# Optimization experiments

Measured on AMD Instinct MI355X. Metric: run time of the kernel, lower is better.

## Reference

```python
import jax, jax.numpy as jnp
import numpy as np

H = 1024
EPS = 1e-5
N_ENT = 1000
TOP_K = 5


def _ln(x, g, b):
    mu = jnp.mean(x, axis=-1, keepdims=True)
    var = jnp.mean((x - mu) ** 2, axis=-1, keepdims=True)
    return (x - mu) * jax.lax.rsqrt(var + EPS) * g + b


def _gelu(x):
    return jax.nn.gelu(x, approximate=False)  # torch nn.GELU default (erf)


def setup_inputs() -> dict:
    key = jax.random.key(0)
    ks = jax.random.split(key, 24)
    s = 0.02
    inp = {
        'hidden_states': jax.random.normal(ks[0], (8, 2048, H), jnp.float32),
        'entity_embeddings': jax.random.normal(ks[1], (N_ENT, H), jnp.float32) * 0.01,
        # entity_encoder: H -> 2H -> H -> LN
        'ee_w1': jax.random.normal(ks[2], (H, 2 * H), jnp.float32) * s,
        'ee_b1': jnp.zeros((2 * H,), jnp.float32),
        'ee_w2': jax.random.normal(ks[3], (2 * H, H), jnp.float32) * s,
        'ee_b2': jnp.zeros((H,), jnp.float32),
        'ee_g': jnp.ones((H,), jnp.float32),
        'ee_beta': jnp.zeros((H,), jnp.float32),
        # relation_encoder: H -> H -> H -> LN
        're_w1': jax.random.normal(ks[4], (H, H), jnp.float32) * s,
        're_b1': jnp.zeros((H,), jnp.float32),
        're_w2': jax.random.normal(ks[5], (H, H), jnp.float32) * s,
        're_b2': jnp.zeros((H,), jnp.float32),
        're_g': jnp.ones((H,), jnp.float32),
        're_beta': jnp.zeros((H,), jnp.float32),
        # reasoning_network: 3H -> 2H -> H -> LN
        'rn_w1': jax.random.normal(ks[6], (3 * H, 2 * H), jnp.float32) * s,
        'rn_b1': jnp.zeros((2 * H,), jnp.float32),
        'rn_w2': jax.random.normal(ks[7], (2 * H, H), jnp.float32) * s,
        'rn_b2': jnp.zeros((H,), jnp.float32),
        'rn_g': jnp.ones((H,), jnp.float32),
        'rn_beta': jnp.zeros((H,), jnp.float32),
        # validation_network: H -> H/2 -> 1 -> sigmoid
        'vn_w1': jax.random.normal(ks[8], (H, H // 2), jnp.float32) * s,
        'vn_b1': jnp.zeros((H // 2,), jnp.float32),
        'vn_w2': jax.random.normal(ks[9], (H // 2, 1), jnp.float32) * s,
        'vn_b2': jnp.zeros((1,), jnp.float32),
    }
    return inp


def reference(hidden_states, entity_embeddings,
              ee_w1, ee_b1, ee_w2, ee_b2, ee_g, ee_beta,
              re_w1, re_b1, re_w2, re_b2, re_g, re_beta,
              rn_w1, rn_b1, rn_w2, rn_b2, rn_g, rn_beta,
              vn_w1, vn_b1, vn_w2, vn_b2):
    # entity encoder over all tokens: [B,S,H]
    entity_features = _ln(_gelu(hidden_states @ ee_w1 + ee_b1) @ ee_w2 + ee_b2, ee_g, ee_beta)

    # query=None path: relation encoder on mean-pooled hidden states [B,H]
    pooled = jnp.mean(hidden_states, axis=1)
    relation_features = _ln(_gelu(pooled @ re_w1 + re_b1) @ re_w2 + re_b2, re_g, re_beta)
    query_features = relation_features

    # similarity + top-k entity retrieval
    entity_similarities = query_features @ entity_embeddings.T  # [B, N_ENT]
    top_values, top_indices = jax.lax.top_k(entity_similarities, TOP_K)
    retrieved_entities = entity_embeddings[top_indices]  # [B, K, H]

    # reasoning input: [mean retrieved entity | relation | mean context]
    entity_vec = jnp.mean(retrieved_entities, axis=1)  # [B,H]
    context_vec = jnp.mean(hidden_states, axis=1)      # [B,H]
    reasoning_in = jnp.concatenate([entity_vec, relation_features, context_vec], axis=-1)  # [B,3H]
    reasoning_output = _ln(_gelu(reasoning_in @ rn_w1 + rn_b1) @ rn_w2 + rn_b2, rn_g, rn_beta)

    validation_scores = jax.nn.sigmoid(_gelu(reasoning_output @ vn_w1 + vn_b1) @ vn_w2 + vn_b2)

    return (entity_features, relation_features, retrieved_entities,
            entity_similarities, top_indices, reasoning_output, validation_scores)
```

## Files before the change

kernel.cpp:

```cpp
#include <hip/hip_runtime.h>
#include <math.h>

#define H 1024
#define SEQ 2048
#define BATCH 8
#define N_ENT 1000
#define TOPK 5
#define LN_EPS 1e-5f

using bf16x8 = __attribute__((ext_vector_type(8))) __bf16;
using f32x4  = __attribute__((ext_vector_type(4))) float;
#define AS1 __attribute__((address_space(1)))
#define AS3 __attribute__((address_space(3)))


__device__ __forceinline__ float gelu_fast(float x) {
    float z = fabsf(x) * 0.70710678118654752440f;
    float t = __builtin_amdgcn_rcpf(fmaf(0.3275911f, z, 1.0f));
    float p = fmaf(fmaf(fmaf(fmaf(1.061405429f, t, -1.453152027f), t, 1.421413741f),
                        t, -0.284496736f), t, 0.254829592f) * t;
    float e = __builtin_amdgcn_exp2f(-z * z * 1.44269504088896f);
    float erfz = fmaf(-p, e, 1.0f);
    float s = copysignf(erfz, x);
    return 0.5f * x * (1.0f + s);
}

__device__ __forceinline__ float sigmoidf_(float x) {
    return 1.0f / (1.0f + expf(-x));
}

__device__ __forceinline__ unsigned short f2bf(float f) {
    unsigned int u = __float_as_uint(f);
    unsigned int r = (u + 0x7fffu + ((u >> 16) & 1u)) >> 16;
    return (unsigned short)r;
}

__device__ float block_sum(float v, float* red) {
    for (int off = 32; off > 0; off >>= 1) v += __shfl_down(v, off, 64);
    int wid = threadIdx.x >> 6;
    int lane = threadIdx.x & 63;
    int nw = blockDim.x >> 6;
    if (lane == 0) red[wid] = v;
    __syncthreads();
    if (threadIdx.x == 0) {
        float s = 0.f;
        for (int i = 0; i < nw; ++i) s += red[i];
        red[0] = s;
    }
    __syncthreads();
    float r = red[0];
    __syncthreads();
    return r;
}


__global__ void f2bf_kernel(const float* __restrict__ in, unsigned short* __restrict__ out, int n) {
    int i = (blockIdx.x * blockDim.x + threadIdx.x) * 4;
    if (i >= n) return;
    float4 v = *(const float4*)(in + i);
    ushort4 o;
    o.x = f2bf(v.x); o.y = f2bf(v.y); o.z = f2bf(v.z); o.w = f2bf(v.w);
    *(ushort4*)(out + i) = o;
}

__global__ void transpose_both_kernel(const float* __restrict__ w1, unsigned short* __restrict__ o1,
                                      const float* __restrict__ w2, unsigned short* __restrict__ o2) {
    __shared__ float tile[32][33];
    int bid = blockIdx.x;
    const float* in; unsigned short* out; int R, C, bx, by;
    if (bid < 2048) { in = w1; out = o1; R = 1024; C = 2048; bx = bid & 63; by = bid >> 6; }
    else { bid -= 2048; in = w2; out = o2; R = 2048; C = 1024; bx = bid & 31; by = bid >> 5; }
    int c0 = bx * 32, r0 = by * 32;
    int tx = threadIdx.x & 31, ty = threadIdx.x >> 5;
#pragma unroll
    for (int i = 0; i < 32; i += 8)
        tile[ty + i][tx] = in[(size_t)(r0 + ty + i) * C + c0 + tx];
    __syncthreads();
#pragma unroll
    for (int i = 0; i < 32; i += 8)
        out[(size_t)(c0 + ty + i) * R + r0 + tx] = f2bf(tile[tx][ty + i]);
}


__global__ void pool1_kernel(const float* __restrict__ hs, float* __restrict__ part,
                             unsigned short* __restrict__ hsb) {
    int sc = blockIdx.x, b = blockIdx.y, t = threadIdx.x;
    size_t rowbase = (size_t)b * SEQ + sc * 64;
    const float* p = hs + rowbase * H + t * 4;
    float4 a = {0.f, 0.f, 0.f, 0.f};
    for (int s = 0; s < 64; ++s) {
        float4 v = *(const float4*)(p + (size_t)s * H);
        a.x += v.x; a.y += v.y; a.z += v.z; a.w += v.w;
        if (hsb) {
            ushort4 o;
            o.x = f2bf(v.x); o.y = f2bf(v.y); o.z = f2bf(v.z); o.w = f2bf(v.w);
            *(ushort4*)(hsb + (rowbase + s) * H + t * 4) = o;
        }
    }
    *(float4*)(part + ((size_t)b * 32 + sc) * H + t * 4) = a;
}

__global__ void pool2_kernel(const float* __restrict__ part, float* __restrict__ pooled) {
    int b = blockIdx.x, t = threadIdx.x;
    float4 s = {0.f, 0.f, 0.f, 0.f};
    for (int sc = 0; sc < 32; ++sc) {
        float4 v = *(const float4*)(part + ((size_t)b * 32 + sc) * H + t * 4);
        s.x += v.x; s.y += v.y; s.z += v.z; s.w += v.w;
    }
    float4 o = {s.x * (1.0f / SEQ), s.y * (1.0f / SEQ), s.z * (1.0f / SEQ), s.w * (1.0f / SEQ)};
    *(float4*)(pooled + (size_t)b * H + t * 4) = o;
}


template <int KRANGE>
__global__ void mlp_partial_kernel(const float* __restrict__ X, int ldx,
                                   const float* __restrict__ W, int N,
                                   float* __restrict__ part) {
    __shared__ float xs[8][KRANGE];
    int jb = blockIdx.x, ks = blockIdx.y, t = threadIdx.x;
    int k0 = ks * KRANGE;
    for (int i = t; i < 8 * KRANGE; i += 256) {
        int b = i / KRANGE, k = i % KRANGE;
        xs[b][k] = X[(size_t)b * ldx + k0 + k];
    }
    __syncthreads();
    int j = jb * 256 + t;
    float acc[8] = {};
    for (int k = 0; k < KRANGE; ++k) {
        float w = W[(size_t)(k0 + k) * N + j];
#pragma unroll
        for (int b = 0; b < 8; ++b) acc[b] = fmaf(xs[b][k], w, acc[b]);
    }
#pragma unroll
    for (int b = 0; b < 8; ++b) part[((size_t)(ks * 8 + b)) * N + j] = acc[b];
}

template <int KRANGE>
__global__ void mlp_partial_fused_kernel(const float* __restrict__ Pprev, int ldp, int nksp,
                                         const float* __restrict__ b1,
                                         const float* __restrict__ W, int N,
                                         float* __restrict__ part) {
    __shared__ float xs[8][KRANGE];
    int jb = blockIdx.x, ks = blockIdx.y, t = threadIdx.x;
    int k0 = ks * KRANGE;
    for (int i = t; i < 8 * KRANGE; i += 256) {
        int b = i / KRANGE, k = i % KRANGE;
        int col = k0 + k;
        float s = b1[col];
        for (int q = 0; q < nksp; ++q) s += Pprev[((size_t)(q * 8 + b)) * ldp + col];
        xs[b][k] = gelu_fast(s);
    }
    __syncthreads();
    int j = jb * 256 + t;
    float acc[8] = {};
    for (int k = 0; k < KRANGE; ++k) {
        float w = W[(size_t)(k0 + k) * N + j];
#pragma unroll
        for (int b = 0; b < 8; ++b) acc[b] = fmaf(xs[b][k], w, acc[b]);
    }
#pragma unroll
    for (int b = 0; b < 8; ++b) part[((size_t)(ks * 8 + b)) * N + j] = acc[b];
}

__global__ void mlp_reduce_ln_kernel(const float* __restrict__ part, const float* __restrict__ bias,
                                     const float* __restrict__ g, const float* __restrict__ be,
                                     float* __restrict__ out, int nks) {
    __shared__ float red[32];
    int b = blockIdx.x, t = threadIdx.x;
    float s = bias[t];
    for (int ks = 0; ks < nks; ++ks) s += part[((size_t)(ks * 8 + b)) * H + t];
    float mu = block_sum(s, red) * (1.0f / H);
    float d = s - mu;
    float var = block_sum(d * d, red) * (1.0f / H);
    out[(size_t)b * H + t] = d * rsqrtf(var + LN_EPS) * g[t] + be[t];
}


__global__ void sim_kernel(const float* __restrict__ rel, const float* __restrict__ ent,
                           float* __restrict__ sims) {
    __shared__ float rl[8 * H];
    int t = threadIdx.x;
    for (int i = t; i < 8 * H; i += 256) rl[i] = rel[i];
    __syncthreads();
    int e = blockIdx.x * 4 + (t >> 6);
    int lane = t & 63;
    float ev[16];
    const float* ep = ent + (size_t)e * H;
#pragma unroll
    for (int i = 0; i < 16; ++i) ev[i] = ep[lane + i * 64];
#pragma unroll
    for (int b = 0; b < 8; ++b) {
        float a = 0.f;
#pragma unroll
        for (int i = 0; i < 16; ++i) a = fmaf(ev[i], rl[b * H + lane + i * 64], a);
        for (int off = 32; off > 0; off >>= 1) a += __shfl_down(a, off, 64);
        if (lane == 0) sims[b * N_ENT + e] = a;
    }
}

__global__ void topk_kernel(const float* __restrict__ sims, float* __restrict__ out_idx_f,
                            int* __restrict__ idx_i) {
    __shared__ float v[1024];
    __shared__ float rv[4];
    __shared__ int ri[4];
    int b = blockIdx.x, t = threadIdx.x;
    for (int i = t; i < 1024; i += 256) v[i] = (i < N_ENT) ? sims[b * N_ENT + i] : -INFINITY;
    __syncthreads();
    for (int k = 0; k < TOPK; ++k) {
        float best = -INFINITY;
        int bi = 0x7fffffff;
        for (int i = t; i < 1024; i += 256) {
            float x = v[i];
            if (x > best || (x == best && i < bi)) { best = x; bi = i; }
        }
        for (int off = 32; off > 0; off >>= 1) {
            float ov = __shfl_down(best, off, 64);
            int oi = __shfl_down(bi, off, 64);
            if (ov > best || (ov == best && oi < bi)) { best = ov; bi = oi; }
        }
        if ((t & 63) == 0) { rv[t >> 6] = best; ri[t >> 6] = bi; }
        __syncthreads();
        if (t == 0) {
            for (int w = 1; w < 4; ++w)
                if (rv[w] > rv[0] || (rv[w] == rv[0] && ri[w] < ri[0])) { rv[0] = rv[w]; ri[0] = ri[w]; }
            int sel = ri[0];
            out_idx_f[b * TOPK + k] = (float)sel;
            idx_i[b * TOPK + k] = sel;
            v[sel] = -INFINITY;
        }
        __syncthreads();
    }
}

__global__ void gather_concat_kernel(const float* __restrict__ ent, const int* __restrict__ idx,
                                     const float* __restrict__ rel, const float* __restrict__ pooled,
                                     float* __restrict__ retrieved, float* __restrict__ xin) {
    int b = blockIdx.x, h = threadIdx.x;
    float acc = 0.f;
    for (int k = 0; k < TOPK; ++k) {
        float v = ent[(size_t)idx[b * TOPK + k] * H + h];
        retrieved[((size_t)b * TOPK + k) * H + h] = v;
        acc += v;
    }
    float* xb = xin + (size_t)b * 3 * H;
    xb[h] = acc * (1.0f / TOPK);
    xb[H + h] = rel[b * H + h];
    xb[2 * H + h] = pooled[b * H + h];
}

__global__ void vn_final_kernel(const float* __restrict__ part, const float* __restrict__ b1,
                                const float* __restrict__ w2, const float* __restrict__ b2,
                                float* __restrict__ vs, int nks) {
    __shared__ float red[32];
    int b = blockIdx.x, t = threadIdx.x;
    float s = b1[t];
    for (int ks = 0; ks < nks; ++ks) s += part[((size_t)(ks * 8 + b)) * 512 + t];
    float c = gelu_fast(s) * w2[t];
    float tot = block_sum(c, red);
    if (t == 0) vs[b] = sigmoidf_(tot + b2[0]);
}

template <int GELU_BF16_OUT>
__global__ __launch_bounds__(512, 2) void gemm256_8ph(const unsigned short* __restrict__ A,
                                                      const unsigned short* __restrict__ Bt,
                                                      const float* __restrict__ bias,
                                                      void* __restrict__ Cout,
                                                      int M, int N, int K) {
    __shared__ __align__(16) unsigned short smem[65536];
    unsigned short (*As)[8192] = (unsigned short(*)[8192])smem;
    unsigned short (*Bs)[8192] = (unsigned short(*)[8192])(smem + 32768);
    const int tid = threadIdx.x;
    const int lane = tid & 63;
    const int w = tid >> 6;
    const int wm2 = w >> 2;
    const int wn4 = w & 3;

    const int Np = N >> 8;
    const int nwg = gridDim.x;
    int bid = blockIdx.x;
    int s = bid;
    if ((nwg & 7) == 0) s = (bid & 7) * (nwg >> 3) + (bid >> 3);
    const int m0 = (s / Np) << 8;
    const int n0 = (s % Np) << 8;

    const int nT = K >> 6;

    const int l7 = lane & 7;
    const int lrow0 = w * 16 + (lane >> 3);
    const int lrow1 = lrow0 + 8;
    const int kel0 = ((l7 ^ (lrow0 & 7)) << 3);
    const int kel1 = ((l7 ^ (lrow1 & 7)) << 3);
    const unsigned short* pa0 = A + (size_t)(m0 + lrow0) * K + kel0;
    const unsigned short* pa1 = A + (size_t)(m0 + lrow1) * K + kel1;
    const unsigned short* pb0 = Bt + (size_t)(n0 + lrow0) * K + kel0;
    const unsigned short* pb1 = Bt + (size_t)(n0 + lrow1) * K + kel1;
    const size_t halfstep = (size_t)128 * K;
    const int dst0 = (w * 16) * 64;
    const int dst1 = dst0 + 8 * 64;

    auto stageA = [&](int t, int half) {
        if (t >= nT) return;
        int slot = (2 * t + half) & 3;
        int koff = t << 6;
        __builtin_amdgcn_global_load_lds((AS1 void*)(pa0 + half * halfstep + koff),
                                         (AS3 void*)(&As[slot][dst0]), 16, 0, 0);
        __builtin_amdgcn_global_load_lds((AS1 void*)(pa1 + half * halfstep + koff),
                                         (AS3 void*)(&As[slot][dst1]), 16, 0, 0);
    };
    auto stageB = [&](int t, int half) {
        if (t >= nT) return;
        int slot = (2 * t + half) & 3;
        int koff = t << 6;
        __builtin_amdgcn_global_load_lds((AS1 void*)(pb0 + half * halfstep + koff),
                                         (AS3 void*)(&Bs[slot][dst0]), 16, 0, 0);
        __builtin_amdgcn_global_load_lds((AS1 void*)(pb1 + half * halfstep + koff),
                                         (AS3 void*)(&Bs[slot][dst1]), 16, 0, 0);
    };

    const int arow = lane & 15;
    const int xk0 = (((lane >> 4) << 4)) ^ (l7 << 4);
    const int xk1 = (64 + ((lane >> 4) << 4)) ^ (l7 << 4);
    auto ldf = [&](const unsigned short* slotbase, int rowbase, int xk) -> bf16x8 {
        return *(const bf16x8*)((const char*)slotbase + (rowbase + arow) * 128 + xk);
    };

    f32x4 acc[8][4] = {};

    stageA(0, 0); stageA(0, 1); stageB(0, 0); stageB(0, 1);
    asm volatile("s_waitcnt vmcnt(4)" ::: "memory");
    stageA(1, 0); stageB(1, 0); stageB(1, 1);
    asm volatile("s_waitcnt vmcnt(6)" ::: "memory");
    __builtin_amdgcn_s_barrier();

    bf16x8 af0[4][2], af1[4][2], bf0[2][2], bf1[2][2];

    for (int T = 0; T < nT; ++T) {
        const unsigned short* Aslot0 = As[(2 * T) & 3];
        const unsigned short* Aslot1 = As[(2 * T + 1) & 3];
        const unsigned short* Bslot0 = Bs[(2 * T) & 3];
        const unsigned short* Bslot1 = Bs[(2 * T + 1) & 3];

#pragma unroll
        for (int ii = 0; ii < 4; ++ii) {
            af0[ii][0] = ldf(Aslot0, ii * 32 + wm2 * 16, xk0);
            af0[ii][1] = ldf(Aslot0, ii * 32 + wm2 * 16, xk1);
        }
#pragma unroll
        for (int jj = 0; jj < 2; ++jj) {
            bf0[jj][0] = ldf(Bslot0, jj * 64 + wn4 * 16, xk0);
            bf0[jj][1] = ldf(Bslot0, jj * 64 + wn4 * 16, xk1);
        }
        stageA(T + 1, 1);
        __builtin_amdgcn_s_barrier();
        __builtin_amdgcn_s_setprio(1);
#pragma unroll
        for (int ii = 0; ii < 4; ++ii)
#pragma unroll
            for (int jj = 0; jj < 2; ++jj) {
                acc[ii][jj] = __builtin_amdgcn_mfma_f32_16x16x32_bf16(af0[ii][0], bf0[jj][0], acc[ii][jj], 0, 0, 0);
                acc[ii][jj] = __builtin_amdgcn_mfma_f32_16x16x32_bf16(af0[ii][1], bf0[jj][1], acc[ii][jj], 0, 0, 0);
            }
        __builtin_amdgcn_s_setprio(0);
        __builtin_amdgcn_s_barrier();

#pragma unroll
        for (int jj = 0; jj < 2; ++jj) {
            bf1[jj][0] = ldf(Bslot1, jj * 64 + wn4 * 16, xk0);
            bf1[jj][1] = ldf(Bslot1, jj * 64 + wn4 * 16, xk1);
        }
        stageA(T + 2, 0);
        __builtin_amdgcn_s_barrier();
        __builtin_amdgcn_s_setprio(1);
#pragma unroll
        for (int ii = 0; ii < 4; ++ii)
#pragma unroll
            for (int jj = 0; jj < 2; ++jj) {
                acc[ii][2 + jj] = __builtin_amdgcn_mfma_f32_16x16x32_bf16(af0[ii][0], bf1[jj][0], acc[ii][2 + jj], 0, 0, 0);
                acc[ii][2 + jj] = __builtin_amdgcn_mfma_f32_16x16x32_bf16(af0[ii][1], bf1[jj][1], acc[ii][2 + jj], 0, 0, 0);
            }
        __builtin_amdgcn_s_setprio(0);
        __builtin_amdgcn_s_barrier();

#pragma unroll
        for (int ii = 0; ii < 4; ++ii) {
            af1[ii][0] = ldf(Aslot1, ii * 32 + wm2 * 16, xk0);
            af1[ii][1] = ldf(Aslot1, ii * 32 + wm2 * 16, xk1);
        }
        stageB(T + 2, 0);
        __builtin_amdgcn_s_barrier();
        __builtin_amdgcn_s_setprio(1);
#pragma unroll
        for (int ii = 0; ii < 4; ++ii)
#pragma unroll
            for (int jj = 0; jj < 2; ++jj) {
                acc[4 + ii][jj] = __builtin_amdgcn_mfma_f32_16x16x32_bf16(af1[ii][0], bf0[jj][0], acc[4 + ii][jj], 0, 0, 0);
                acc[4 + ii][jj] = __builtin_amdgcn_mfma_f32_16x16x32_bf16(af1[ii][1], bf0[jj][1], acc[4 + ii][jj], 0, 0, 0);
            }
        __builtin_amdgcn_s_setprio(0);
        __builtin_amdgcn_s_barrier();

        stageB(T + 2, 1);
        if (T + 3 <= nT) {
            asm volatile("s_waitcnt vmcnt(6)" ::: "memory");
        } else {
            asm volatile("s_waitcnt vmcnt(0)" ::: "memory");
        }
        __builtin_amdgcn_s_barrier();
        __builtin_amdgcn_s_setprio(1);
#pragma unroll
        for (int ii = 0; ii < 4; ++ii)
#pragma unroll
            for (int jj = 0; jj < 2; ++jj) {
                acc[4 + ii][2 + jj] = __builtin_amdgcn_mfma_f32_16x16x32_bf16(af1[ii][0], bf1[jj][0], acc[4 + ii][2 + jj], 0, 0, 0);
                acc[4 + ii][2 + jj] = __builtin_amdgcn_mfma_f32_16x16x32_bf16(af1[ii][1], bf1[jj][1], acc[4 + ii][2 + jj], 0, 0, 0);
            }
        __builtin_amdgcn_s_setprio(0);
        __builtin_amdgcn_s_barrier();
    }

    const int cn = lane & 15;
    const int rbase = (lane >> 4) * 4;
    __syncthreads();

    if (GELU_BF16_OUT) {
#pragma unroll
        for (int i = 0; i < 8; ++i) {
            int lr = (i >> 2) * 128 + (i & 3) * 32 + wm2 * 16 + rbase;
#pragma unroll
            for (int j = 0; j < 4; ++j) {
                int nl = (j >> 1) * 128 + (j & 1) * 64 + wn4 * 16 + cn;
                float bv = bias[n0 + nl];
#pragma unroll
                for (int r = 0; r < 4; ++r) {
                    float c = gelu_fast(acc[i][j][r] + bv);
                    int row = lr + r;
                    int byte = (row << 9) + (nl << 1);
                    byte ^= (row & 7) << 4;
                    *(unsigned short*)((char*)smem + byte) = f2bf(c);
                }
            }
        }
        __syncthreads();
#pragma unroll
        for (int u = 0; u < 16; ++u) {
            int off = u * 8192 + tid * 16;
            int row = off >> 9, colb = off & 511;
            int src = off ^ ((row & 7) << 4);
            *(int4*)((char*)Cout + ((size_t)(m0 + row) * N + n0) * 2 + colb) =
                *(const int4*)((const char*)smem + src);
        }
    } else {
        float* smf = (float*)smem;
#pragma unroll
        for (int p = 0; p < 2; ++p) {
            if (p) __syncthreads();
#pragma unroll
            for (int ii = 0; ii < 4; ++ii) {
                int i = p * 4 + ii;
                int lr = (i & 3) * 32 + wm2 * 16 + rbase;
#pragma unroll
                for (int j = 0; j < 4; ++j) {
                    int nl = (j >> 1) * 128 + (j & 1) * 64 + wn4 * 16 + cn;
                    float bv = bias[n0 + nl];
#pragma unroll
                    for (int r = 0; r < 4; ++r) {
                        int row = lr + r;
                        int byte = (row << 10) + (nl << 2);
                        byte ^= (row & 7) << 4;
                        *(float*)((char*)smf + byte) = acc[p * 4 + ii][j][r] + bv;
                    }
                }
            }
            __syncthreads();
#pragma unroll
            for (int u = 0; u < 16; ++u) {
                int off = u * 8192 + tid * 16;
                int row = off >> 10, colb = off & 1023;
                int src = off ^ ((row & 7) << 4);
                *(int4*)((char*)Cout + ((size_t)(m0 + p * 128 + row) * N + n0) * 4 + colb) =
                    *(const int4*)((const char*)smf + src);
            }
        }
    }
}

__global__ void ln_rows_kernel(float* __restrict__ x, const float* __restrict__ g,
                               const float* __restrict__ beta) {
    __shared__ float red[32];
    float* p = x + (size_t)blockIdx.x * H;
    int t = threadIdx.x;
    float4 v = *(const float4*)(p + t * 4);
    float s = v.x + v.y + v.z + v.w;
    float mu = block_sum(s, red) * (1.0f / H);
    float4 d = { v.x - mu, v.y - mu, v.z - mu, v.w - mu };
    float d2 = d.x * d.x + d.y * d.y + d.z * d.z + d.w * d.w;
    float var = block_sum(d2, red) * (1.0f / H);
    float inv = rsqrtf(var + LN_EPS);
    float4 gg = *(const float4*)(g + t * 4);
    float4 bb = *(const float4*)(beta + t * 4);
    float4 o = { d.x * inv * gg.x + bb.x, d.y * inv * gg.y + bb.y,
                 d.z * inv * gg.z + bb.z, d.w * inv * gg.w + bb.w };
    *(float4*)(p + t * 4) = o;
}


extern "C" void kernel_launch(void* const* d_in, const int* in_sizes, int n_in,
                              void* d_out, int out_size, void* d_ws, size_t ws_size,
                              hipStream_t stream) {
    const float* hs     = (const float*)d_in[0];
    const float* ent    = (const float*)d_in[1];
    const float* ee_w1  = (const float*)d_in[2];
    const float* ee_b1  = (const float*)d_in[3];
    const float* ee_w2  = (const float*)d_in[4];
    const float* ee_b2  = (const float*)d_in[5];
    const float* ee_g   = (const float*)d_in[6];
    const float* ee_be  = (const float*)d_in[7];
    const float* re_w1  = (const float*)d_in[8];
    const float* re_b1  = (const float*)d_in[9];
    const float* re_w2  = (const float*)d_in[10];
    const float* re_b2  = (const float*)d_in[11];
    const float* re_g   = (const float*)d_in[12];
    const float* re_be  = (const float*)d_in[13];
    const float* rn_w1  = (const float*)d_in[14];
    const float* rn_b1  = (const float*)d_in[15];
    const float* rn_w2  = (const float*)d_in[16];
    const float* rn_b2  = (const float*)d_in[17];
    const float* rn_g   = (const float*)d_in[18];
    const float* rn_be  = (const float*)d_in[19];
    const float* vn_w1  = (const float*)d_in[20];
    const float* vn_b1  = (const float*)d_in[21];
    const float* vn_w2  = (const float*)d_in[22];
    const float* vn_b2  = (const float*)d_in[23];

    float* out = (float*)d_out;
    float* ef   = out;
    float* rel  = ef + (size_t)BATCH * SEQ * H;
    float* retr = rel + BATCH * H;
    float* sims = retr + BATCH * TOPK * H;
    float* tidx = sims + BATCH * N_ENT;
    float* ro   = tidx + BATCH * TOPK;
    float* vs   = ro + BATCH * H;

    float* ws = (float*)d_ws;
    size_t o = 0;
    float* pooled = ws + o; o += 8192;
    int*   idx_i  = (int*)(ws + o); o += 64;
    float* xin    = ws + o; o += 8 * 3 * H;
    float* partA  = ws + o; o += 48 * 8 * 2048;
    float* partB  = ws + o; o += 32 * 8 * 1024;
    unsigned short* w1t = (unsigned short*)(ws + o); o += (2048 * 1024) / 2;
    unsigned short* w2t = (unsigned short*)(ws + o); o += (2048 * 1024) / 2;
    unsigned short* hsb = (unsigned short*)(ws + o);

    long long avail = (long long)(ws_size / 4) - (long long)o;
    int chunk = (int)(avail / 1536);
    chunk &= ~255;
    int total = BATCH * SEQ;
    if (chunk > total) chunk = total;
    if (chunk < 256) chunk = 256;
    bool full = (chunk >= total);
    unsigned short* midb = hsb + (size_t)chunk * H;

    pool1_kernel<<<dim3(32, BATCH), 256, 0, stream>>>(hs, partA, full ? hsb : nullptr);

    transpose_both_kernel<<<4096, 256, 0, stream>>>(ee_w1, w1t, ee_w2, w2t);

    pool2_kernel<<<BATCH, 256, 0, stream>>>(partA, pooled);

    mlp_partial_kernel<32><<<dim3(4, 32), 256, 0, stream>>>(pooled, H, re_w1, H, partA);
    mlp_partial_fused_kernel<32><<<dim3(4, 32), 256, 0, stream>>>(partA, H, 32, re_b1,
                                                                  re_w2, H, partB);
    mlp_reduce_ln_kernel<<<BATCH, 1024, 0, stream>>>(partB, re_b2, re_g, re_be, rel, 32);

    sim_kernel<<<250, 256, 0, stream>>>(rel, ent, sims);
    topk_kernel<<<BATCH, 256, 0, stream>>>(sims, tidx, idx_i);
    gather_concat_kernel<<<BATCH, 1024, 0, stream>>>(ent, idx_i, rel, pooled, retr, xin);

    mlp_partial_kernel<64><<<dim3(8, 48), 256, 0, stream>>>(xin, 3 * H, rn_w1, 2 * H, partA);
    mlp_partial_fused_kernel<64><<<dim3(4, 32), 256, 0, stream>>>(partA, 2 * H, 48, rn_b1,
                                                                  rn_w2, H, partB);
    mlp_reduce_ln_kernel<<<BATCH, 1024, 0, stream>>>(partB, rn_b2, rn_g, rn_be, ro, 32);

    mlp_partial_kernel<64><<<dim3(2, 16), 256, 0, stream>>>(ro, H, vn_w1, 512, partA);
    vn_final_kernel<<<BATCH, 512, 0, stream>>>(partA, vn_b1, vn_w2, vn_b2, vs, 16);

    for (int r0 = 0; r0 < total; r0 += chunk) {
        int m = total - r0;
        if (m > chunk) m = chunk;
        if (!full) {
            int nconv = m * H;
            f2bf_kernel<<<(nconv / 4 + 255) / 256, 256, 0, stream>>>(hs + (size_t)r0 * H, hsb, nconv);
        }
        unsigned short* a1 = full ? (hsb + (size_t)r0 * H) : hsb;
        gemm256_8ph<1><<<(m / 256) * (2048 / 256), 512, 0, stream>>>(a1, w1t, ee_b1, midb,
                                                                     m, 2048, 1024);
        gemm256_8ph<0><<<(m / 256) * (1024 / 256), 512, 0, stream>>>(midb, w2t, ee_b2,
                                                                     ef + (size_t)r0 * H,
                                                                     m, 1024, 2048);
    }
    ln_rows_kernel<<<total, 256, 0, stream>>>(ef, ee_g, ee_be);
}
```

Baseline: 534.5 us.

## Rework GEMM waitcnt schedule, drop LDS-staged epilogue, double pool1 grid

The pooling kernel now uses 64 sequence chunks of 32 rows instead of 32 chunks of 64, with an unrolled loop and a branch hoisted out of it, to put more blocks in flight on the memory-bound read of hidden states. In the bf16 GEMM, prologue loads are reordered and the vmcnt waits are spread across the phase barriers instead of sitting in one place. The epilogue now writes results straight from registers to global memory rather than staging them through swizzled LDS for coalesced 16-byte stores. That removes LDS traffic and syncs, but the stores become scattered scalar writes, and the moved waitcnt counts could be wrong.

Measured after the change: 498.2 us. 1.07x faster.

```diff
diff --git a/kernel.cpp b/kernel.cpp
--- a/kernel.cpp
+++ b/kernel.cpp
@@ -85,26 +85,33 @@
 __global__ void pool1_kernel(const float* __restrict__ hs, float* __restrict__ part,
                              unsigned short* __restrict__ hsb) {
     int sc = blockIdx.x, b = blockIdx.y, t = threadIdx.x;
-    size_t rowbase = (size_t)b * SEQ + sc * 64;
+    size_t rowbase = (size_t)b * SEQ + sc * 32;
     const float* p = hs + rowbase * H + t * 4;
     float4 a = {0.f, 0.f, 0.f, 0.f};
-    for (int s = 0; s < 64; ++s) {
-        float4 v = *(const float4*)(p + (size_t)s * H);
-        a.x += v.x; a.y += v.y; a.z += v.z; a.w += v.w;
-        if (hsb) {
+    if (hsb) {
+#pragma unroll 4
+        for (int s = 0; s < 32; ++s) {
+            float4 v = *(const float4*)(p + (size_t)s * H);
+            a.x += v.x; a.y += v.y; a.z += v.z; a.w += v.w;
             ushort4 o;
             o.x = f2bf(v.x); o.y = f2bf(v.y); o.z = f2bf(v.z); o.w = f2bf(v.w);
             *(ushort4*)(hsb + (rowbase + s) * H + t * 4) = o;
         }
-    }
-    *(float4*)(part + ((size_t)b * 32 + sc) * H + t * 4) = a;
+    } else {
+#pragma unroll 4
+        for (int s = 0; s < 32; ++s) {
+            float4 v = *(const float4*)(p + (size_t)s * H);
+            a.x += v.x; a.y += v.y; a.z += v.z; a.w += v.w;
+        }
+    }
+    *(float4*)(part + ((size_t)b * 64 + sc) * H + t * 4) = a;
 }
 
 __global__ void pool2_kernel(const float* __restrict__ part, float* __restrict__ pooled) {
     int b = blockIdx.x, t = threadIdx.x;
     float4 s = {0.f, 0.f, 0.f, 0.f};
-    for (int sc = 0; sc < 32; ++sc) {
-        float4 v = *(const float4*)(part + ((size_t)b * 32 + sc) * H + t * 4);
+    for (int sc = 0; sc < 64; ++sc) {
+        float4 v = *(const float4*)(part + ((size_t)b * 64 + sc) * H + t * 4);
         s.x += v.x; s.y += v.y; s.z += v.z; s.w += v.w;
     }
     float4 o = {s.x * (1.0f / SEQ), s.y * (1.0f / SEQ), s.z * (1.0f / SEQ), s.w * (1.0f / SEQ)};
@@ -266,9 +273,8 @@
                                                       const float* __restrict__ bias,
                                                       void* __restrict__ Cout,
                                                       int M, int N, int K) {
-    __shared__ __align__(16) unsigned short smem[65536];
-    unsigned short (*As)[8192] = (unsigned short(*)[8192])smem;
-    unsigned short (*Bs)[8192] = (unsigned short(*)[8192])(smem + 32768);
+    __shared__ __align__(16) unsigned short As[4][128 * 64];
+    __shared__ __align__(16) unsigned short Bs[4][128 * 64];
     const int tid = threadIdx.x;
     const int lane = tid & 63;
     const int w = tid >> 6;
@@ -326,10 +332,9 @@
 
     f32x4 acc[8][4] = {};
 
-    stageA(0, 0); stageA(0, 1); stageB(0, 0); stageB(0, 1);
-    asm volatile("s_waitcnt vmcnt(4)" ::: "memory");
+    stageA(0, 0); stageB(0, 0); stageA(0, 1); stageB(0, 1);
     stageA(1, 0); stageB(1, 0); stageB(1, 1);
-    asm volatile("s_waitcnt vmcnt(6)" ::: "memory");
+    asm volatile("s_waitcnt vmcnt(10)" ::: "memory");
     __builtin_amdgcn_s_barrier();
 
     bf16x8 af0[4][2], af1[4][2], bf0[2][2], bf1[2][2];
@@ -361,6 +366,8 @@
                 acc[ii][jj] = __builtin_amdgcn_mfma_f32_16x16x32_bf16(af0[ii][1], bf0[jj][1], acc[ii][jj], 0, 0, 0);
             }
         __builtin_amdgcn_s_setprio(0);
+        if (T == 0) asm volatile("s_waitcnt vmcnt(8)" ::: "memory");
+        else        asm volatile("s_waitcnt vmcnt(10)" ::: "memory");
         __builtin_amdgcn_s_barrier();
 
 #pragma unroll
@@ -379,6 +386,8 @@
                 acc[ii][2 + jj] = __builtin_amdgcn_mfma_f32_16x16x32_bf16(af0[ii][1], bf1[jj][1], acc[ii][2 + jj], 0, 0, 0);
             }
         __builtin_amdgcn_s_setprio(0);
+        if (T + 2 >= nT) asm volatile("s_waitcnt vmcnt(8)" ::: "memory");
+        else             asm volatile("s_waitcnt vmcnt(10)" ::: "memory");
         __builtin_amdgcn_s_barrier();
 
 #pragma unroll
@@ -400,11 +409,6 @@
         __builtin_amdgcn_s_barrier();
 
         stageB(T + 2, 1);
-        if (T + 3 <= nT) {
-            asm volatile("s_waitcnt vmcnt(6)" ::: "memory");
-        } else {
-            asm volatile("s_waitcnt vmcnt(0)" ::: "memory");
-        }
         __builtin_amdgcn_s_barrier();
         __builtin_amdgcn_s_setprio(1);
 #pragma unroll
@@ -415,70 +419,29 @@
                 acc[4 + ii][2 + jj] = __builtin_amdgcn_mfma_f32_16x16x32_bf16(af1[ii][1], bf1[jj][1], acc[4 + ii][2 + jj], 0, 0, 0);
             }
         __builtin_amdgcn_s_setprio(0);
+        if (T + 2 < nT) asm volatile("s_waitcnt vmcnt(10)" ::: "memory");
+        else            asm volatile("s_waitcnt vmcnt(0)" ::: "memory");
         __builtin_amdgcn_s_barrier();
     }
 
     const int cn = lane & 15;
     const int rbase = (lane >> 4) * 4;
-    __syncthreads();
-
-    if (GELU_BF16_OUT) {
-#pragma unroll
-        for (int i = 0; i < 8; ++i) {
-            int lr = (i >> 2) * 128 + (i & 3) * 32 + wm2 * 16 + rbase;
-#pragma unroll
-            for (int j = 0; j < 4; ++j) {
-                int nl = (j >> 1) * 128 + (j & 1) * 64 + wn4 * 16 + cn;
-                float bv = bias[n0 + nl];
-#pragma unroll
-                for (int r = 0; r < 4; ++r) {
-                    float c = gelu_fast(acc[i][j][r] + bv);
-                    int row = lr + r;
-                    int byte = (row << 9) + (nl << 1);
-                    byte ^= (row & 7) << 4;
-                    *(unsigned short*)((char*)smem + byte) = f2bf(c);
+#pragma unroll
+    for (int i = 0; i < 8; ++i) {
+        int mbase = m0 + (i >> 2) * 128 + (i & 3) * 32 + wm2 * 16 + rbase;
+#pragma unroll
+        for (int j = 0; j < 4; ++j) {
+            int n = n0 + (j >> 1) * 128 + (j & 1) * 64 + wn4 * 16 + cn;
+            float bv = bias[n];
+#pragma unroll
+            for (int r = 0; r < 4; ++r) {
+                float c = acc[i][j][r] + bv;
+                if (GELU_BF16_OUT) {
+                    c = gelu_fast(c);
+                    ((unsigned short*)Cout)[(size_t)(mbase + r) * N + n] = f2bf(c);
+                } else {
+                    ((float*)Cout)[(size_t)(mbase + r) * N + n] = c;
                 }
-            }
-        }
-        __syncthreads();
-#pragma unroll
-        for (int u = 0; u < 16; ++u) {
-            int off = u * 8192 + tid * 16;
-            int row = off >> 9, colb = off & 511;
-            int src = off ^ ((row & 7) << 4);
-            *(int4*)((char*)Cout + ((size_t)(m0 + row) * N + n0) * 2 + colb) =
-                *(const int4*)((const char*)smem + src);
-        }
-    } else {
-        float* smf = (float*)smem;
-#pragma unroll
-        for (int p = 0; p < 2; ++p) {
-            if (p) __syncthreads();
-#pragma unroll
-            for (int ii = 0; ii < 4; ++ii) {
-                int i = p * 4 + ii;
-                int lr = (i & 3) * 32 + wm2 * 16 + rbase;
-#pragma unroll
-                for (int j = 0; j < 4; ++j) {
-                    int nl = (j >> 1) * 128 + (j & 1) * 64 + wn4 * 16 + cn;
-                    float bv = bias[n0 + nl];
-#pragma unroll
-                    for (int r = 0; r < 4; ++r) {
-                        int row = lr + r;
-                        int byte = (row << 10) + (nl << 2);
-                        byte ^= (row & 7) << 4;
-                        *(float*)((char*)smf + byte) = acc[p * 4 + ii][j][r] + bv;
-                    }
-                }
-            }
-            __syncthreads();
-#pragma unroll
-            for (int u = 0; u < 16; ++u) {
-                int off = u * 8192 + tid * 16;
-                int row = off >> 10, colb = off & 1023;
-                int src = off ^ ((row & 7) << 4);
-                *(int4*)((char*)Cout + ((size_t)(m0 + p * 128 + row) * N + n0) * 4 + colb) =
-                    *(const int4*)((const char*)smf + src);
             }
         }
     }
@@ -561,7 +524,7 @@
     bool full = (chunk >= total);
     unsigned short* midb = hsb + (size_t)chunk * H;
 
-    pool1_kernel<<<dim3(32, BATCH), 256, 0, stream>>>(hs, partA, full ? hsb : nullptr);
+    pool1_kernel<<<dim3(64, BATCH), 256, 0, stream>>>(hs, partA, full ? hsb : nullptr);
 
     transpose_both_kernel<<<4096, 256, 0, stream>>>(ee_w1, w1t, ee_w2, w2t);
 
```
